# Kernel tuning notes

Hardware: AMD Instinct MI355X
Metric: run time of the kernel (lower is better)

Reference implementation:

```python
import jax, jax.numpy as jnp
import numpy as np

BINS = 256
H = 2048
N = 2_000_000


def _tensor2image(x):
    # standard GAN denorm: [-1,1] -> [0,1]
    return (x + 1.0) * 0.5


def _cdf(vals):
    # torch.histc(bins=256, min=0, max=256): unit-width bins, values in [0,255]
    idx = jnp.clip(jnp.floor(vals), 0, BINS - 1).astype(jnp.int32)
    hist = jnp.zeros((BINS,), jnp.float32).at[idx].add(1.0)
    return jnp.cumsum(hist) / hist.sum()


def _trans_table(ref_cdf, adj_cdf):
    # cal_trans: for i in 1..255, first j in 1..255 with adj[j-1] <= ref[i] <= adj[j]
    i_vals = ref_cdf[1:]  # [255]
    cond = (adj_cdf[:-1][None, :] <= i_vals[:, None]) & (i_vals[:, None] <= adj_cdf[1:][None, :])  # [255,255]
    found = cond.any(axis=1)
    first_j = jnp.argmax(cond, axis=1) + 1
    tab = jnp.where(found, first_j, jnp.arange(1, BINS))  # unmatched entries keep identity
    tab = jnp.concatenate([jnp.zeros((1,), tab.dtype), tab])
    tab = tab.at[BINS - 1].set(BINS - 1)
    return tab.astype(jnp.float32)


def _hist_match(dst_img, ref_img, i0, i1, i2, i3):
    # dst_img, ref_img: [3,H,W]; indices: [N]
    dst_align = dst_img[:, i0, i1]  # [3,N]
    ref_align = ref_img[:, i2, i3]  # [3,N]
    cdf_dst = jax.vmap(_cdf)(dst_align)  # [3,256]
    cdf_ref = jax.vmap(_cdf)(ref_align)  # [3,256]
    tables = jax.vmap(_trans_table)(cdf_dst, cdf_ref)  # [3,256]
    bins = jnp.clip(dst_align, 0, BINS - 1).astype(jnp.int32)  # int() truncation on [0,255]
    new_align = jnp.take_along_axis(tables, bins, axis=1)  # [3,N]
    return dst_img.at[:, i0, i1].set(new_align)


def reference(input_data, target_data, mask_src, mask_tar, index0, index1, index2, index3, ref_data):
    inp = _tensor2image(input_data) * 255.0
    tgt = _tensor2image(target_data) * 255.0
    ref = _tensor2image(ref_data) * 255.0
    h = mask_src.shape[2]
    m_src = jnp.broadcast_to(mask_src, (1, 3, h, h))
    m_tar = jnp.broadcast_to(mask_tar, (1, 3, h, h))
    input_masked = inp * m_src
    target_masked = (tgt * m_tar)[0]  # [3,H,W]
    ref_masked = (ref * m_src)[0]     # [3,H,W]
    i0, i1, i2, i3 = index0[0], index1[0], index2[0], index3[0]
    matched = _hist_match(ref_masked, target_masked, i0, i1, i2, i3)[None]  # [1,3,H,W]
    input_match = jax.lax.stop_gradient(matched) * m_src  # no_grad in original
    return jnp.mean((input_masked - input_match) ** 2)


def setup_inputs() -> dict:
    key = jax.random.key(0)
    ks = jax.random.split(key, 9)
    inp = {
        "input_data": jax.random.uniform(ks[0], (1, 3, H, H), jnp.float32, -1.0, 1.0),
        "target_data": jax.random.uniform(ks[1], (1, 3, H, H), jnp.float32, -1.0, 1.0),
        "mask_src": (jax.random.uniform(ks[2], (1, 1, H, H)) > 0.5).astype(jnp.float32),
        "mask_tar": (jax.random.uniform(ks[3], (1, 1, H, H)) > 0.5).astype(jnp.float32),
        "index0": jax.random.randint(ks[4], (1, N), 0, H, jnp.int32),
        "index1": jax.random.randint(ks[5], (1, N), 0, H, jnp.int32),
        "index2": jax.random.randint(ks[6], (1, N), 0, H, jnp.int32),
        "index3": jax.random.randint(ks[7], (1, N), 0, H, jnp.int32),
        "ref_data": jax.random.uniform(ks[8], (1, 3, H, H), jnp.float32, -1.0, 1.0),
    }
    return inp
```

## Files before the change

### kernel.cpp

```cpp
#include <hip/hip_runtime.h>

#define HDIM 2048
#define HH (HDIM * HDIM)
#define NIDX 2000000
#define BINS 256
#define NCOPY 16
#define TL_BLOCKS 2048
#define NCHUNK 2000
#define CH_I4 250
#define NWIN 64

#define PART_OFF   0
#define TAB_OFF    16384
#define WGL_OFF    20480
#define HIST_OFF   24576
#define CNT_D_OFF  131072
#define CNT_R_OFF  393216
#define OFF_D_OFF  655360
#define OFF_R_OFF  1179648
#define FLAGS_OFF  2097152
#define SORT_D_OFF 6291456
#define SORT_R_OFF 10485760

__global__ __launch_bounds__(256) void prep_kernel(
    const int* __restrict__ i0, const int* __restrict__ i1,
    const int* __restrict__ i2, const int* __restrict__ i3,
    unsigned* __restrict__ hist, unsigned* __restrict__ flags32,
    unsigned short* __restrict__ cnt_d, unsigned short* __restrict__ cnt_r)
{
    __shared__ unsigned cntd[NWIN], cntr[NWIN];
    const int t = threadIdx.x;
    const int gtid = blockIdx.x * 256 + t;
    const int stride = gridDim.x * 256;

    for (int k = gtid; k < NCOPY * 6 * BINS; k += stride) hist[k] = 0;
    for (int k = gtid; k < HH / 4; k += stride) flags32[k] = 0;

    if (blockIdx.x < NCHUNK) {
        if (t < NWIN) { cntd[t] = 0; cntr[t] = 0; }
        __syncthreads();
        if (t < CH_I4) {
            const int q = blockIdx.x * CH_I4 + t;
            const int4 a = ((const int4*)i0)[q];
            const int4 b = ((const int4*)i1)[q];
            const int4 c = ((const int4*)i2)[q];
            const int4 d = ((const int4*)i3)[q];
            const int pd[4] = {a.x * HDIM + b.x, a.y * HDIM + b.y, a.z * HDIM + b.z, a.w * HDIM + b.w};
            const int pr[4] = {c.x * HDIM + d.x, c.y * HDIM + d.y, c.z * HDIM + d.z, c.w * HDIM + d.w};
#pragma unroll
            for (int k = 0; k < 4; k++) atomicAdd(&cntd[pd[k] >> 16], 1u);
#pragma unroll
            for (int k = 0; k < 4; k++) atomicAdd(&cntr[pr[k] >> 16], 1u);
        }
        __syncthreads();
        if (t < NWIN) {
            cnt_d[blockIdx.x * NWIN + t] = (unsigned short)cntd[t];
            cnt_r[blockIdx.x * NWIN + t] = (unsigned short)cntr[t];
        }
    }
}

__global__ __launch_bounds__(1024) void off_kernel(
    const unsigned short* __restrict__ cnt_d, const unsigned short* __restrict__ cnt_r,
    unsigned* __restrict__ off_d, unsigned* __restrict__ off_r, unsigned* __restrict__ Wg)
{
    __shared__ unsigned psum[16][NWIN];
    __shared__ unsigned segbase[16][NWIN];
    __shared__ unsigned Wl[NWIN + 1];
    const int t = threadIdx.x;
    const int w = t & 63, seg = t >> 6;

    for (int side = 0; side < 2; side++) {
        const unsigned short* cnt = side ? cnt_r : cnt_d;
        unsigned* off = side ? off_r : off_d;
        unsigned s = 0;
        for (int b = seg * 125; b < seg * 125 + 125; b++) s += cnt[b * NWIN + w];
        psum[seg][w] = s;
        __syncthreads();
        if (t < NWIN) {
            unsigned run = 0;
            for (int sg = 0; sg < 16; sg++) { segbase[sg][t] = run; run += psum[sg][t]; }
            unsigned inc = run;
            for (int d = 1; d < 64; d <<= 1) {
                const unsigned y = __shfl_up(inc, d, 64);
                if (t >= d) inc += y;
            }
            Wl[t] = inc - run;
            if (t == 63) Wl[64] = inc;
        }
        __syncthreads();
        unsigned run = Wl[w] + segbase[seg][w];
        for (int b = seg * 125; b < seg * 125 + 125; b++) {
            off[b * NWIN + w] = run;
            run += cnt[b * NWIN + w];
        }
        if (t < NWIN + 1) Wg[side * (NWIN + 1) + t] = Wl[t];
        __syncthreads();
    }
}

__global__ __launch_bounds__(256) void place_kernel(
    const int* __restrict__ i0, const int* __restrict__ i1,
    const int* __restrict__ i2, const int* __restrict__ i3,
    const unsigned* __restrict__ off_d, const unsigned* __restrict__ off_r,
    unsigned short* __restrict__ sorted_d, unsigned short* __restrict__ sorted_r)
{
    __shared__ unsigned cur[NWIN];
    const int b = blockIdx.x;
    const int t = threadIdx.x;

    if (t < NWIN) cur[t] = off_d[b * NWIN + t];
    __syncthreads();
    if (t < CH_I4) {
        const int q = b * CH_I4 + t;
        const int4 a = ((const int4*)i0)[q];
        const int4 bb = ((const int4*)i1)[q];
        const int pd[4] = {a.x * HDIM + bb.x, a.y * HDIM + bb.y, a.z * HDIM + bb.z, a.w * HDIM + bb.w};
#pragma unroll
        for (int k = 0; k < 4; k++) {
            const unsigned pos = atomicAdd(&cur[pd[k] >> 16], 1u);
            sorted_d[pos] = (unsigned short)(pd[k] & 0xFFFF);
        }
    }
    __syncthreads();
    if (t < NWIN) cur[t] = off_r[b * NWIN + t];
    __syncthreads();
    if (t < CH_I4) {
        const int q = b * CH_I4 + t;
        const int4 c = ((const int4*)i2)[q];
        const int4 d = ((const int4*)i3)[q];
        const int pr[4] = {c.x * HDIM + d.x, c.y * HDIM + d.y, c.z * HDIM + d.z, c.w * HDIM + d.w};
#pragma unroll
        for (int k = 0; k < 4; k++) {
            const unsigned pos = atomicAdd(&cur[pr[k] >> 16], 1u);
            sorted_r[pos] = (unsigned short)(pr[k] & 0xFFFF);
        }
    }
}

__global__ __launch_bounds__(256) void whist_kernel(
    const float* __restrict__ ref, const float* __restrict__ tgt,
    const float* __restrict__ msrc, const float* __restrict__ mtar,
    const unsigned short* __restrict__ sorted_d, const unsigned short* __restrict__ sorted_r,
    const unsigned* __restrict__ Wg,
    unsigned char* __restrict__ flags, unsigned* __restrict__ hist)
{
    __shared__ unsigned lhist[6 * BINS];
    __shared__ unsigned Ws[2 * (NWIN + 1)];
    const int t = threadIdx.x;
    for (int k = t; k < 6 * BINS; k += 256) lhist[k] = 0;
    if (t < 2 * (NWIN + 1)) Ws[t] = Wg[t];
    __syncthreads();

    unsigned z0 = 0, z1 = 0, z2 = 0, z3 = 0, z4 = 0, z5 = 0;
    const int cls = blockIdx.x & 7;
    const int bc  = blockIdx.x >> 3;
    const int cstep = 256 * 256;

    for (int w = cls; w < NWIN; w += 8) {
        const int base = w << 16;
        const int e0 = (int)Ws[w], e1 = (int)Ws[w + 1];
        for (int e = e0 + bc * 256 + t; e < e1; e += cstep) {
            const int pd = base | (int)sorted_d[e];
            const float mm = msrc[pd];
            const float v0 = ref[pd], v1 = ref[HH + pd], v2 = ref[2 * HH + pd];
            flags[pd] = 1;
            const float f0 = ((v0 + 1.0f) * 0.5f) * 255.0f * mm;
            const float f1 = ((v1 + 1.0f) * 0.5f) * 255.0f * mm;
            const float f2 = ((v2 + 1.0f) * 0.5f) * 255.0f * mm;
            const unsigned b0 = (unsigned)(int)fminf(fmaxf(floorf(f0), 0.0f), 255.0f);
            const unsigned b1 = (unsigned)(int)fminf(fmaxf(floorf(f1), 0.0f), 255.0f);
            const unsigned b2 = (unsigned)(int)fminf(fmaxf(floorf(f2), 0.0f), 255.0f);
            if (b0) atomicAdd(&lhist[           b0], 1u); else z0++;
            if (b1) atomicAdd(&lhist[1 * BINS + b1], 1u); else z1++;
            if (b2) atomicAdd(&lhist[2 * BINS + b2], 1u); else z2++;
        }
    }
    for (int w = cls; w < NWIN; w += 8) {
        const int base = w << 16;
        const int e0 = (int)Ws[NWIN + 1 + w], e1 = (int)Ws[NWIN + 1 + w + 1];
        for (int e = e0 + bc * 256 + t; e < e1; e += cstep) {
            const int pr = base | (int)sorted_r[e];
            const float mm = mtar[pr];
            const float v0 = tgt[pr], v1 = tgt[HH + pr], v2 = tgt[2 * HH + pr];
            const float f0 = ((v0 + 1.0f) * 0.5f) * 255.0f * mm;
            const float f1 = ((v1 + 1.0f) * 0.5f) * 255.0f * mm;
            const float f2 = ((v2 + 1.0f) * 0.5f) * 255.0f * mm;
            const unsigned b0 = (unsigned)(int)fminf(fmaxf(floorf(f0), 0.0f), 255.0f);
            const unsigned b1 = (unsigned)(int)fminf(fmaxf(floorf(f1), 0.0f), 255.0f);
            const unsigned b2 = (unsigned)(int)fminf(fmaxf(floorf(f2), 0.0f), 255.0f);
            if (b0) atomicAdd(&lhist[3 * BINS + b0], 1u); else z3++;
            if (b1) atomicAdd(&lhist[4 * BINS + b1], 1u); else z4++;
            if (b2) atomicAdd(&lhist[5 * BINS + b2], 1u); else z5++;
        }
    }

    if (z0) atomicAdd(&lhist[0 * BINS], z0);
    if (z1) atomicAdd(&lhist[1 * BINS], z1);
    if (z2) atomicAdd(&lhist[2 * BINS], z2);
    if (z3) atomicAdd(&lhist[3 * BINS], z3);
    if (z4) atomicAdd(&lhist[4 * BINS], z4);
    if (z5) atomicAdd(&lhist[5 * BINS], z5);
    __syncthreads();
    unsigned* h = hist + (blockIdx.x & (NCOPY - 1)) * (6 * BINS);
    for (int k = t; k < 6 * BINS; k += 256) {
        const unsigned v = lhist[k];
        if (v) atomicAdd(&h[k], v);
    }
}

__global__ __launch_bounds__(256) void table_kernel(
    const unsigned* __restrict__ hist, float* __restrict__ tabg)
{
    __shared__ float    cdf[6 * BINS];
    __shared__ unsigned wsum[4];

    const int t    = threadIdx.x;
    const int lane = t & 63;
    const int wid  = t >> 6;

    for (int ch = 0; ch < 6; ch++) {
        unsigned x = 0;
#pragma unroll
        for (int cp = 0; cp < NCOPY; cp++) x += hist[cp * (6 * BINS) + ch * BINS + t];
#pragma unroll
        for (int d = 1; d < 64; d <<= 1) {
            const unsigned y = __shfl_up(x, d, 64);
            if (lane >= d) x += y;
        }
        if (lane == 63) wsum[wid] = x;
        __syncthreads();
        unsigned prefix = 0;
        for (int w = 0; w < wid; w++) prefix += wsum[w];
        x += prefix;
        cdf[ch * BINS + t] = (float)x / 2000000.0f;
        __syncthreads();
    }
    for (int c = 0; c < 3; c++) {
        float o;
        if (t == 0)             o = 0.0f;
        else if (t == BINS - 1) o = 255.0f;
        else {
            const float v = cdf[c * BINS + t];
            const float* arr = cdf + (3 + c) * BINS;
            int lo = 0, hi = 256;
            while (lo < hi) { const int mid = (lo + hi) >> 1; if (arr[mid] < v) lo = mid + 1; else hi = mid; }
            const int J0 = ((lo > 1) ? lo : 1) - 1;
            int lo2 = 0, hi2 = 256;
            while (lo2 < hi2) { const int mid = (lo2 + hi2) >> 1; if (arr[mid] <= v) lo2 = mid + 1; else hi2 = mid; }
            const int J1 = ((lo2 - 1) < 254 ? (lo2 - 1) : 254);
            const bool found = (lo2 >= 1) && (J0 <= J1);
            o = found ? (float)(J0 + 1) : (float)t;
        }
        tabg[c * BINS + t] = o;
    }
}

__global__ __launch_bounds__(256) void tabloss_kernel(
    const float* __restrict__ inp, const float* __restrict__ ref,
    const float* __restrict__ msrc, const float* __restrict__ tabg,
    const unsigned char* __restrict__ flags, double* __restrict__ partials)
{
    __shared__ float  tab[3 * BINS];
    __shared__ double red[256];

    const int t = threadIdx.x;
    for (int k = t; k < 3 * BINS; k += 256) tab[k] = tabg[k];
    __syncthreads();

    double local = 0.0;
    const int stride = gridDim.x * 256;
    for (int g = blockIdx.x * 256 + t; g < HH / 4; g += stride) {
        const int p = g * 4;
        const float4 mv = *(const float4*)(msrc + p);
        const uchar4 fw = *(const uchar4*)(flags + p);
        const unsigned samp[4] = {fw.x, fw.y, fw.z, fw.w};
        const float m[4] = {mv.x, mv.y, mv.z, mv.w};
#pragma unroll
        for (int c = 0; c < 3; c++) {
            const float4 rv = *(const float4*)(ref + c * HH + p);
            const float4 iv = *(const float4*)(inp + c * HH + p);
            const float r[4] = {rv.x, rv.y, rv.z, rv.w};
            const float x4[4] = {iv.x, iv.y, iv.z, iv.w};
            float s = 0.0f;
#pragma unroll
            for (int k = 0; k < 4; k++) {
                const float mm = m[k];
                const float refm = ((r[k] + 1.0f) * 0.5f) * 255.0f * mm;
                const float inpm = ((x4[k] + 1.0f) * 0.5f) * 255.0f * mm;
                float matchv;
                if (samp[k]) {
                    const int bidx = (int)fminf(fmaxf(refm, 0.0f), 255.0f);
                    matchv = tab[c * BINS + bidx];
                } else {
                    matchv = refm;
                }
                const float dd = inpm - matchv * mm;
                s += dd * dd;
            }
            local += (double)s;
        }
    }
    red[t] = local;
    __syncthreads();
    for (int s2 = 128; s2 > 0; s2 >>= 1) {
        if (t < s2) red[t] += red[t + s2];
        __syncthreads();
    }
    if (t == 0) partials[blockIdx.x] = red[0];
}

__global__ __launch_bounds__(256) void finalize_kernel(
    const double* __restrict__ partials, float* __restrict__ out)
{
    const int t = threadIdx.x;
    double s = 0.0;
    for (int k = t; k < TL_BLOCKS; k += 256) s += partials[k];
    __shared__ double red[256];
    red[t] = s;
    __syncthreads();
    for (int s2 = 128; s2 > 0; s2 >>= 1) {
        if (t < s2) red[t] += red[t + s2];
        __syncthreads();
    }
    if (t == 0) out[0] = (float)(red[0] / (double)(3 * HH));
}

extern "C" void kernel_launch(void* const* d_in, const int* in_sizes, int n_in,
                              void* d_out, int out_size, void* d_ws, size_t ws_size,
                              hipStream_t stream)
{
    const float* input_data  = (const float*)d_in[0];
    const float* target_data = (const float*)d_in[1];
    const float* mask_src    = (const float*)d_in[2];
    const float* mask_tar    = (const float*)d_in[3];
    const int*   i0          = (const int*)d_in[4];
    const int*   i1          = (const int*)d_in[5];
    const int*   i2          = (const int*)d_in[6];
    const int*   i3          = (const int*)d_in[7];
    const float* ref_data    = (const float*)d_in[8];
    float* out = (float*)d_out;

    char* ws = (char*)d_ws;
    double*         partials = (double*)(ws + PART_OFF);
    float*          tabg     = (float*)(ws + TAB_OFF);
    unsigned*       Wg       = (unsigned*)(ws + WGL_OFF);
    unsigned*       hist     = (unsigned*)(ws + HIST_OFF);
    unsigned short* cnt_d    = (unsigned short*)(ws + CNT_D_OFF);
    unsigned short* cnt_r    = (unsigned short*)(ws + CNT_R_OFF);
    unsigned*       off_d    = (unsigned*)(ws + OFF_D_OFF);
    unsigned*       off_r    = (unsigned*)(ws + OFF_R_OFF);
    unsigned*       flags32  = (unsigned*)(ws + FLAGS_OFF);
    unsigned char*  flags    = (unsigned char*)(ws + FLAGS_OFF);
    unsigned short* sorted_d = (unsigned short*)(ws + SORT_D_OFF);
    unsigned short* sorted_r = (unsigned short*)(ws + SORT_R_OFF);

    prep_kernel<<<2048, 256, 0, stream>>>(i0, i1, i2, i3, hist, flags32, cnt_d, cnt_r);
    off_kernel<<<1, 1024, 0, stream>>>(cnt_d, cnt_r, off_d, off_r, Wg);
    place_kernel<<<NCHUNK, 256, 0, stream>>>(i0, i1, i2, i3, off_d, off_r, sorted_d, sorted_r);
    whist_kernel<<<2048, 256, 0, stream>>>(ref_data, target_data, mask_src, mask_tar,
                                           sorted_d, sorted_r, Wg, flags, hist);
    table_kernel<<<1, 256, 0, stream>>>(hist, tabg);
    tabloss_kernel<<<TL_BLOCKS, 256, 0, stream>>>(input_data, ref_data, mask_src, tabg,
                                                  flags, partials);
    finalize_kernel<<<1, 256, 0, stream>>>(partials, out);
}
```

Measured before the change: 395.3 us.

## Replace scattered histogram gathers with per-window occurrence counts and dense streaming

Index pairs are now flattened once into linear pixel arrays, which place_kernel reuses. Windows shrink to 32K pixels and each histogram block builds packed 8-bit occurrence counters in shared memory, then streams the image, mask and flags for its window densely with float4 loads, weighting each pixel by its count. This replaces random gathers of 2M pixels with coalesced reads, and the flag array is written in full, so it no longer needs clearing. The cost is extra writes and reads of the flattened index arrays, and the 8-bit counters would overflow if one pixel were indexed more than 255 times.

```diff
diff --git a/kernel.cpp b/kernel.cpp
--- a/kernel.cpp
+++ b/kernel.cpp
@@ -6,9 +6,9 @@
 #define BINS 256
 #define NCOPY 16
 #define TL_BLOCKS 2048
-#define NCHUNK 2000
-#define CH_I4 250
-#define NWIN 64
+#define NCHUNK 1000
+#define CH_I4 500
+#define NWIN 128
 
 #define PART_OFF   0
 #define TAB_OFF    16384
@@ -21,42 +21,41 @@
 #define FLAGS_OFF  2097152
 #define SORT_D_OFF 6291456
 #define SORT_R_OFF 10485760
-
-__global__ __launch_bounds__(256) void prep_kernel(
+#define PD_OFF     14680064
+#define PR_OFF     23068672
+
+__global__ __launch_bounds__(256) void flat_kernel(
     const int* __restrict__ i0, const int* __restrict__ i1,
     const int* __restrict__ i2, const int* __restrict__ i3,
-    unsigned* __restrict__ hist, unsigned* __restrict__ flags32,
+    int* __restrict__ pdArr, int* __restrict__ prArr,
     unsigned short* __restrict__ cnt_d, unsigned short* __restrict__ cnt_r)
 {
     __shared__ unsigned cntd[NWIN], cntr[NWIN];
-    const int t = threadIdx.x;
-    const int gtid = blockIdx.x * 256 + t;
-    const int stride = gridDim.x * 256;
-
-    for (int k = gtid; k < NCOPY * 6 * BINS; k += stride) hist[k] = 0;
-    for (int k = gtid; k < HH / 4; k += stride) flags32[k] = 0;
-
-    if (blockIdx.x < NCHUNK) {
-        if (t < NWIN) { cntd[t] = 0; cntr[t] = 0; }
-        __syncthreads();
-        if (t < CH_I4) {
-            const int q = blockIdx.x * CH_I4 + t;
-            const int4 a = ((const int4*)i0)[q];
-            const int4 b = ((const int4*)i1)[q];
-            const int4 c = ((const int4*)i2)[q];
-            const int4 d = ((const int4*)i3)[q];
-            const int pd[4] = {a.x * HDIM + b.x, a.y * HDIM + b.y, a.z * HDIM + b.z, a.w * HDIM + b.w};
-            const int pr[4] = {c.x * HDIM + d.x, c.y * HDIM + d.y, c.z * HDIM + d.z, c.w * HDIM + d.w};
-#pragma unroll
-            for (int k = 0; k < 4; k++) atomicAdd(&cntd[pd[k] >> 16], 1u);
-#pragma unroll
-            for (int k = 0; k < 4; k++) atomicAdd(&cntr[pr[k] >> 16], 1u);
-        }
-        __syncthreads();
-        if (t < NWIN) {
-            cnt_d[blockIdx.x * NWIN + t] = (unsigned short)cntd[t];
-            cnt_r[blockIdx.x * NWIN + t] = (unsigned short)cntr[t];
-        }
+    const int b = blockIdx.x, t = threadIdx.x;
+    for (int k = t; k < NWIN; k += 256) { cntd[k] = 0; cntr[k] = 0; }
+    __syncthreads();
+
+    for (int i = t; i < CH_I4; i += 256) {
+        const int q = b * CH_I4 + i;
+        const int4 a  = ((const int4*)i0)[q];
+        const int4 bb = ((const int4*)i1)[q];
+        const int4 c  = ((const int4*)i2)[q];
+        const int4 d  = ((const int4*)i3)[q];
+        const int4 pd4 = make_int4(a.x * HDIM + bb.x, a.y * HDIM + bb.y,
+                                   a.z * HDIM + bb.z, a.w * HDIM + bb.w);
+        const int4 pr4 = make_int4(c.x * HDIM + d.x, c.y * HDIM + d.y,
+                                   c.z * HDIM + d.z, c.w * HDIM + d.w);
+        ((int4*)pdArr)[q] = pd4;
+        ((int4*)prArr)[q] = pr4;
+        atomicAdd(&cntd[pd4.x >> 15], 1u); atomicAdd(&cntd[pd4.y >> 15], 1u);
+        atomicAdd(&cntd[pd4.z >> 15], 1u); atomicAdd(&cntd[pd4.w >> 15], 1u);
+        atomicAdd(&cntr[pr4.x >> 15], 1u); atomicAdd(&cntr[pr4.y >> 15], 1u);
+        atomicAdd(&cntr[pr4.z >> 15], 1u); atomicAdd(&cntr[pr4.w >> 15], 1u);
+    }
+    __syncthreads();
+    for (int k = t; k < NWIN; k += 256) {
+        cnt_d[b * NWIN + k] = (unsigned short)cntd[k];
+        cnt_r[b * NWIN + k] = (unsigned short)cntr[k];
     }
 }
 
@@ -64,11 +63,9 @@
     const unsigned short* __restrict__ cnt_d, const unsigned short* __restrict__ cnt_r,
     unsigned* __restrict__ off_d, unsigned* __restrict__ off_r, unsigned* __restrict__ Wg)
 {
-    __shared__ unsigned psum[16][NWIN];
-    __shared__ unsigned segbase[16][NWIN];
-    __shared__ unsigned Wl[NWIN + 1];
+    __shared__ unsigned psum[8][NWIN], segbase[8][NWIN], wtot[NWIN], Wl[NWIN + 1];
     const int t = threadIdx.x;
-    const int w = t & 63, seg = t >> 6;
+    const int w = t & (NWIN - 1), seg = t >> 7;
 
     for (int side = 0; side < 2; side++) {
         const unsigned short* cnt = side ? cnt_r : cnt_d;
@@ -79,20 +76,20 @@
         __syncthreads();
         if (t < NWIN) {
             unsigned run = 0;
-            for (int sg = 0; sg < 16; sg++) { segbase[sg][t] = run; run += psum[sg][t]; }
-            unsigned inc = run;
-            for (int d = 1; d < 64; d <<= 1) {
-                const unsigned y = __shfl_up(inc, d, 64);
-                if (t >= d) inc += y;
-            }
-            Wl[t] = inc - run;
-            if (t == 63) Wl[64] = inc;
-        }
-        __syncthreads();
-        unsigned run = Wl[w] + segbase[seg][w];
+            for (int sg = 0; sg < 8; sg++) { segbase[sg][t] = run; run += psum[sg][t]; }
+            wtot[t] = run;
+        }
+        __syncthreads();
+        if (t == 0) {
+            unsigned run = 0;
+            for (int w2 = 0; w2 < NWIN; w2++) { Wl[w2] = run; run += wtot[w2]; }
+            Wl[NWIN] = run;
+        }
+        __syncthreads();
+        unsigned run2 = Wl[w] + segbase[seg][w];
         for (int b = seg * 125; b < seg * 125 + 125; b++) {
-            off[b * NWIN + w] = run;
-            run += cnt[b * NWIN + w];
+            off[b * NWIN + w] = run2;
+            run2 += cnt[b * NWIN + w];
         }
         if (t < NWIN + 1) Wg[side * (NWIN + 1) + t] = Wl[t];
         __syncthreads();
@@ -100,110 +97,108 @@
 }
 
 __global__ __launch_bounds__(256) void place_kernel(
-    const int* __restrict__ i0, const int* __restrict__ i1,
-    const int* __restrict__ i2, const int* __restrict__ i3,
+    const int* __restrict__ pdArr, const int* __restrict__ prArr,
     const unsigned* __restrict__ off_d, const unsigned* __restrict__ off_r,
     unsigned short* __restrict__ sorted_d, unsigned short* __restrict__ sorted_r)
 {
     __shared__ unsigned cur[NWIN];
-    const int b = blockIdx.x;
-    const int t = threadIdx.x;
-
-    if (t < NWIN) cur[t] = off_d[b * NWIN + t];
-    __syncthreads();
-    if (t < CH_I4) {
-        const int q = b * CH_I4 + t;
-        const int4 a = ((const int4*)i0)[q];
-        const int4 bb = ((const int4*)i1)[q];
-        const int pd[4] = {a.x * HDIM + bb.x, a.y * HDIM + bb.y, a.z * HDIM + bb.z, a.w * HDIM + bb.w};
+    const int b = blockIdx.x, t = threadIdx.x;
+
+    for (int k = t; k < NWIN; k += 256) cur[k] = off_d[b * NWIN + k];
+    __syncthreads();
+    for (int i = t; i < CH_I4; i += 256) {
+        const int4 p4 = ((const int4*)pdArr)[b * CH_I4 + i];
+        const int pd[4] = {p4.x, p4.y, p4.z, p4.w};
 #pragma unroll
         for (int k = 0; k < 4; k++) {
-            const unsigned pos = atomicAdd(&cur[pd[k] >> 16], 1u);
-            sorted_d[pos] = (unsigned short)(pd[k] & 0xFFFF);
-        }
-    }
-    __syncthreads();
-    if (t < NWIN) cur[t] = off_r[b * NWIN + t];
-    __syncthreads();
-    if (t < CH_I4) {
-        const int q = b * CH_I4 + t;
-        const int4 c = ((const int4*)i2)[q];
-        const int4 d = ((const int4*)i3)[q];
-        const int pr[4] = {c.x * HDIM + d.x, c.y * HDIM + d.y, c.z * HDIM + d.z, c.w * HDIM + d.w};
+            const unsigned pos = atomicAdd(&cur[pd[k] >> 15], 1u);
+            sorted_d[pos] = (unsigned short)(pd[k] & 32767);
+        }
+    }
+    __syncthreads();
+    for (int k = t; k < NWIN; k += 256) cur[k] = off_r[b * NWIN + k];
+    __syncthreads();
+    for (int i = t; i < CH_I4; i += 256) {
+        const int4 p4 = ((const int4*)prArr)[b * CH_I4 + i];
+        const int pr[4] = {p4.x, p4.y, p4.z, p4.w};
 #pragma unroll
         for (int k = 0; k < 4; k++) {
-            const unsigned pos = atomicAdd(&cur[pr[k] >> 16], 1u);
-            sorted_r[pos] = (unsigned short)(pr[k] & 0xFFFF);
-        }
-    }
-}
-
-__global__ __launch_bounds__(256) void whist_kernel(
+            const unsigned pos = atomicAdd(&cur[pr[k] >> 15], 1u);
+            sorted_r[pos] = (unsigned short)(pr[k] & 32767);
+        }
+    }
+}
+
+__global__ __launch_bounds__(256) void whist2_kernel(
     const float* __restrict__ ref, const float* __restrict__ tgt,
     const float* __restrict__ msrc, const float* __restrict__ mtar,
     const unsigned short* __restrict__ sorted_d, const unsigned short* __restrict__ sorted_r,
     const unsigned* __restrict__ Wg,
     unsigned char* __restrict__ flags, unsigned* __restrict__ hist)
 {
-    __shared__ unsigned lhist[6 * BINS];
-    __shared__ unsigned Ws[2 * (NWIN + 1)];
-    const int t = threadIdx.x;
-    for (int k = t; k < 6 * BINS; k += 256) lhist[k] = 0;
-    if (t < 2 * (NWIN + 1)) Ws[t] = Wg[t];
-    __syncthreads();
-
-    unsigned z0 = 0, z1 = 0, z2 = 0, z3 = 0, z4 = 0, z5 = 0;
-    const int cls = blockIdx.x & 7;
-    const int bc  = blockIdx.x >> 3;
-    const int cstep = 256 * 256;
-
-    for (int w = cls; w < NWIN; w += 8) {
-        const int base = w << 16;
-        const int e0 = (int)Ws[w], e1 = (int)Ws[w + 1];
-        for (int e = e0 + bc * 256 + t; e < e1; e += cstep) {
-            const int pd = base | (int)sorted_d[e];
-            const float mm = msrc[pd];
-            const float v0 = ref[pd], v1 = ref[HH + pd], v2 = ref[2 * HH + pd];
-            flags[pd] = 1;
-            const float f0 = ((v0 + 1.0f) * 0.5f) * 255.0f * mm;
-            const float f1 = ((v1 + 1.0f) * 0.5f) * 255.0f * mm;
-            const float f2 = ((v2 + 1.0f) * 0.5f) * 255.0f * mm;
+    __shared__ unsigned cnt32[8192];
+    __shared__ unsigned lhist[3 * BINS];
+
+    const int b = blockIdx.x, t = threadIdx.x;
+    const int side = b & 1, half = (b >> 1) & 1, win = b >> 2;
+
+    for (int k = t; k < 8192; k += 256) cnt32[k] = 0;
+    for (int k = t; k < 3 * BINS; k += 256) lhist[k] = 0;
+    __syncthreads();
+
+    const unsigned e0 = Wg[side * (NWIN + 1) + win];
+    const unsigned e1 = Wg[side * (NWIN + 1) + win + 1];
+    const unsigned short* se = side ? sorted_r : sorted_d;
+    for (unsigned e = e0 + t; e < e1; e += 256) {
+        const unsigned lo = se[e];
+        atomicAdd(&cnt32[lo >> 2], 1u << ((lo & 3) * 8));
+    }
+    __syncthreads();
+
+    const float* img = side ? tgt : ref;
+    const float* msk = side ? mtar : msrc;
+    const int P0 = (win << 15) + half * 16384;
+    unsigned z0 = 0, z1 = 0, z2 = 0;
+
+    for (int j = t; j < 4096; j += 256) {
+        const unsigned cw = cnt32[half * 4096 + j];
+        const int p = P0 + j * 4;
+        if (side == 0) {
+            const uchar4 f = make_uchar4((cw & 255u) ? 1 : 0, ((cw >> 8) & 255u) ? 1 : 0,
+                                         ((cw >> 16) & 255u) ? 1 : 0, (cw >> 24) ? 1 : 0);
+            *(uchar4*)(flags + p) = f;
+        }
+        if (cw == 0) continue;
+        const float4 m4 = *(const float4*)(msk + p);
+        const float4 v0 = *(const float4*)(img + p);
+        const float4 v1 = *(const float4*)(img + HH + p);
+        const float4 v2 = *(const float4*)(img + 2 * HH + p);
+        const float m[4]  = {m4.x, m4.y, m4.z, m4.w};
+        const float a0[4] = {v0.x, v0.y, v0.z, v0.w};
+        const float a1[4] = {v1.x, v1.y, v1.z, v1.w};
+        const float a2[4] = {v2.x, v2.y, v2.z, v2.w};
+#pragma unroll
+        for (int k = 0; k < 4; k++) {
+            const unsigned c = (cw >> (k * 8)) & 255u;
+            if (!c) continue;
+            const float mm = m[k];
+            const float f0 = ((a0[k] + 1.0f) * 0.5f) * 255.0f * mm;
+            const float f1 = ((a1[k] + 1.0f) * 0.5f) * 255.0f * mm;
+            const float f2 = ((a2[k] + 1.0f) * 0.5f) * 255.0f * mm;
             const unsigned b0 = (unsigned)(int)fminf(fmaxf(floorf(f0), 0.0f), 255.0f);
             const unsigned b1 = (unsigned)(int)fminf(fmaxf(floorf(f1), 0.0f), 255.0f);
             const unsigned b2 = (unsigned)(int)fminf(fmaxf(floorf(f2), 0.0f), 255.0f);
-            if (b0) atomicAdd(&lhist[           b0], 1u); else z0++;
-            if (b1) atomicAdd(&lhist[1 * BINS + b1], 1u); else z1++;
-            if (b2) atomicAdd(&lhist[2 * BINS + b2], 1u); else z2++;
-        }
-    }
-    for (int w = cls; w < NWIN; w += 8) {
-        const int base = w << 16;
-        const int e0 = (int)Ws[NWIN + 1 + w], e1 = (int)Ws[NWIN + 1 + w + 1];
-        for (int e = e0 + bc * 256 + t; e < e1; e += cstep) {
-            const int pr = base | (int)sorted_r[e];
-            const float mm = mtar[pr];
-            const float v0 = tgt[pr], v1 = tgt[HH + pr], v2 = tgt[2 * HH + pr];
-            const float f0 = ((v0 + 1.0f) * 0.5f) * 255.0f * mm;
-            const float f1 = ((v1 + 1.0f) * 0.5f) * 255.0f * mm;
-            const float f2 = ((v2 + 1.0f) * 0.5f) * 255.0f * mm;
-            const unsigned b0 = (unsigned)(int)fminf(fmaxf(floorf(f0), 0.0f), 255.0f);
-            const unsigned b1 = (unsigned)(int)fminf(fmaxf(floorf(f1), 0.0f), 255.0f);
-            const unsigned b2 = (unsigned)(int)fminf(fmaxf(floorf(f2), 0.0f), 255.0f);
-            if (b0) atomicAdd(&lhist[3 * BINS + b0], 1u); else z3++;
-            if (b1) atomicAdd(&lhist[4 * BINS + b1], 1u); else z4++;
-            if (b2) atomicAdd(&lhist[5 * BINS + b2], 1u); else z5++;
-        }
-    }
-
+            if (b0) atomicAdd(&lhist[           b0], c); else z0 += c;
+            if (b1) atomicAdd(&lhist[1 * BINS + b1], c); else z1 += c;
+            if (b2) atomicAdd(&lhist[2 * BINS + b2], c); else z2 += c;
+        }
+    }
     if (z0) atomicAdd(&lhist[0 * BINS], z0);
     if (z1) atomicAdd(&lhist[1 * BINS], z1);
     if (z2) atomicAdd(&lhist[2 * BINS], z2);
-    if (z3) atomicAdd(&lhist[3 * BINS], z3);
-    if (z4) atomicAdd(&lhist[4 * BINS], z4);
-    if (z5) atomicAdd(&lhist[5 * BINS], z5);
-    __syncthreads();
-    unsigned* h = hist + (blockIdx.x & (NCOPY - 1)) * (6 * BINS);
-    for (int k = t; k < 6 * BINS; k += 256) {
+    __syncthreads();
+    unsigned* h = hist + (b & (NCOPY - 1)) * (6 * BINS) + side * (3 * BINS);
+    for (int k = t; k < 3 * BINS; k += 256) {
         const unsigned v = lhist[k];
         if (v) atomicAdd(&h[k], v);
     }
@@ -350,16 +345,18 @@
     unsigned short* cnt_r    = (unsigned short*)(ws + CNT_R_OFF);
     unsigned*       off_d    = (unsigned*)(ws + OFF_D_OFF);
     unsigned*       off_r    = (unsigned*)(ws + OFF_R_OFF);
-    unsigned*       flags32  = (unsigned*)(ws + FLAGS_OFF);
     unsigned char*  flags    = (unsigned char*)(ws + FLAGS_OFF);
     unsigned short* sorted_d = (unsigned short*)(ws + SORT_D_OFF);
     unsigned short* sorted_r = (unsigned short*)(ws + SORT_R_OFF);
-
-    prep_kernel<<<2048, 256, 0, stream>>>(i0, i1, i2, i3, hist, flags32, cnt_d, cnt_r);
+    int*            pdArr    = (int*)(ws + PD_OFF);
+    int*            prArr    = (int*)(ws + PR_OFF);
+
+    hipMemsetAsync(ws + HIST_OFF, 0, NCOPY * 6 * BINS * 4, stream);
+    flat_kernel<<<NCHUNK, 256, 0, stream>>>(i0, i1, i2, i3, pdArr, prArr, cnt_d, cnt_r);
     off_kernel<<<1, 1024, 0, stream>>>(cnt_d, cnt_r, off_d, off_r, Wg);
-    place_kernel<<<NCHUNK, 256, 0, stream>>>(i0, i1, i2, i3, off_d, off_r, sorted_d, sorted_r);
-    whist_kernel<<<2048, 256, 0, stream>>>(ref_data, target_data, mask_src, mask_tar,
-                                           sorted_d, sorted_r, Wg, flags, hist);
+    place_kernel<<<NCHUNK, 256, 0, stream>>>(pdArr, prArr, off_d, off_r, sorted_d, sorted_r);
+    whist2_kernel<<<4 * NWIN, 256, 0, stream>>>(ref_data, target_data, mask_src, mask_tar,
+                                                sorted_d, sorted_r, Wg, flags, hist);
     table_kernel<<<1, 256, 0, stream>>>(hist, tabg);
     tabloss_kernel<<<TL_BLOCKS, 256, 0, stream>>>(input_data, ref_data, mask_src, tabg,
                                                   flags, partials);
```

After: 342.8 us. 1.15x faster.
